# Kernel optimization log

Hardware: AMD Instinct MI355X
Metric: run time of the kernel (lower is better)

## Reference

```python
import jax, jax.numpy as jnp
import numpy as np
import math

MUL = 16                      # num_in_features == num_out_features
LDIMS = (1, 3, 5)             # 0e, 1o, 2e  (lmax = 2)
FEAT = MUL * sum(LDIMS)       # 144 = irreps dim = number_of_basis
PATHS = [(0,0,0),(1,1,0),(2,2,0),
         (0,1,1),(1,0,1),(1,2,1),(2,1,1),
         (0,2,2),(1,1,2),(2,0,2),(2,2,2)]
DOT_PATHS = [(0,0,0),(1,1,0),(2,2,0)]

# ---------- real Wigner-3j / Clebsch-Gordan (e3nn convention), numpy precompute ----------

def _su2_cg(j1, m1, j2, m2, j3, m3):
    if m3 != m1 + m2:
        return 0.0
    f = math.factorial
    vmin = max(-j1 + j2 + m3, -j1 + m1, 0)
    vmax = min(j2 + j3 + m1, j3 - j1 + j2, j3 + m3)
    C = math.sqrt((2*j3+1) * f(j3+j1-j2) * f(j3-j1+j2) * f(j1+j2-j3)
                  * f(j3+m3) * f(j3-m3)
                  / (f(j1+j2+j3+1) * f(j1-m1) * f(j1+m1) * f(j2-m2) * f(j2+m2)))
    S = 0.0
    for v in range(vmin, vmax + 1):
        S += (-1.0)**(v + j2 + m2) * f(j2+j3+m1-v) * f(j1-m1+v) / (
            f(v) * f(j3-j1+j2-v) * f(j3+m3-v) * f(v+j1-j2-m3))
    return C * S

def _qmat(l):
    # complex -> real spherical-harmonic change of basis (e3nn convention)
    q = np.zeros((2*l+1, 2*l+1), dtype=np.complex128)
    for m in range(-l, 0):
        q[l+m, l+abs(m)] = 1.0/math.sqrt(2)
        q[l+m, l-abs(m)] = -1j/math.sqrt(2)
    q[l, l] = 1.0
    for m in range(1, l+1):
        q[l+m, l+abs(m)] = (-1)**m/math.sqrt(2)
        q[l+m, l-abs(m)] = 1j*(-1)**m/math.sqrt(2)
    return (-1j)**l * q

def _real_w3j(l1, l2, l3):
    C = np.zeros((2*l1+1, 2*l2+1, 2*l3+1))
    for i, m1 in enumerate(range(-l1, l1+1)):
        for j, m2 in enumerate(range(-l2, l2+1)):
            for k, m3 in enumerate(range(-l3, l3+1)):
                C[i, j, k] = _su2_cg(l1, m1, l2, m2, l3, m3)
    Cr = np.einsum('ij,kl,mn,ikn->jlm', _qmat(l1), _qmat(l2),
                   np.conj(_qmat(l3).T), C.astype(np.complex128))
    Cr = np.real(Cr)
    return (Cr / np.linalg.norm(Cr)).astype(np.float32)  # unit Frobenius norm (3j convention)

W3J = {p: _real_w3j(*p) for p in set(PATHS)}

# ---------- fully connected tensor product (component/element normalization) ----------

def _split(x):
    # blocked layout: [mul x 0e | mul x 1o | mul x 2e]
    n = x.shape[0]
    xs, o = [], 0
    for d in LDIMS:
        xs.append(x[:, o:o + MUL*d].reshape(n, MUL, d))
        o += MUL * d
    return xs

def _fctp(x1, x2, W):
    # W: [11, u, v, w] stacked per PATHS
    xs1, xs2 = _split(x1), _split(x2)
    n = x1.shape[0]
    n_paths = {l3: sum(1 for p in PATHS if p[2] == l3) for l3 in range(3)}
    outs = [None, None, None]
    for i, (l1, l2, l3) in enumerate(PATHS):
        C = jnp.asarray(W3J[(l1, l2, l3)])          # [i, j, k]
        scale = math.sqrt((2*l3 + 1) / (n_paths[l3] * MUL * MUL))
        a = jnp.einsum('nvj,ijk->nivk', xs2[l2], C)      # [n, i, v, k]
        b = jnp.einsum('nui,nivk->nuvk', xs1[l1], a)     # [n, u, v, k]
        o = scale * jnp.einsum('nuvk,uvw->nwk', b, W[i]) # [n, w, k]
        outs[l3] = o if outs[l3] is None else outs[l3] + o
    return jnp.concatenate([o.reshape(n, -1) for o in outs], axis=1)  # [n, 9*MUL]

def _dot(x1, x2, Wd):
    # FCTP(irreps_input, irreps_input, '0e'): paths (0,0,0),(1,1,0),(2,2,0), out mul = 1
    xs1, xs2 = _split(x1), _split(x2)
    fan = 3 * MUL * MUL
    acc = 0.0
    for i, (l1, l2, l3) in enumerate(DOT_PATHS):
        C = jnp.asarray(W3J[(l1, l2, l3)])[:, :, 0]      # [i, j]
        t = jnp.einsum('nui,ij,nvj->nuv', xs1[l1], C, xs2[l2])
        acc = acc + jnp.einsum('nuv,uv->n', t, Wd[i])
    return (acc * math.sqrt(1.0 / fan))[:, None]         # [n, 1]

def setup_inputs() -> dict:
    key = jax.random.key(0)
    ks = jax.random.split(key, 8)
    N = 50000
    return {
        'nodes_features': jax.random.normal(ks[0], (N, FEAT), jnp.float32),
        'degree_matrix': jax.random.normal(ks[1], (N,), jnp.float32),
        'edges_features_distance': jax.random.normal(ks[2], (N,), jnp.float32),
        'edges_features_bond': jax.random.normal(ks[3], (N,), jnp.float32),
        'w_q': jax.random.normal(ks[4], (11, MUL, MUL, MUL), jnp.float32),
        'w_k': jax.random.normal(ks[5], (11, MUL, MUL, MUL), jnp.float32),
        'w_v': jax.random.normal(ks[6], (11, MUL, MUL, MUL), jnp.float32),
        'w_dot': jax.random.normal(ks[7], (3, MUL, MUL), jnp.float32),
    }

def reference(nodes_features, degree_matrix, edges_features_distance,
              edges_features_bond, w_q, w_k, w_v, w_dot):
    # degree_matrix / edges_features_* are unused by the original forward
    x = nodes_features
    q = _fctp(x, x, w_q)                   # tp_q(x, x)
    k = _fctp(x, x, w_k)                   # tp_k(x, x)
    v = _fctp(x, x, w_v)                   # tp(x, x)
    d = _dot(q, k, w_dot)                  # [n, 1]
    e = jnp.exp(d / math.sqrt(float(FEAT)))
    attn = e / (e + 1e-10)                 # sum over last dim of size 1 + eps
    out = attn * v                         # dropout is identity in eval mode
    out = out.reshape(-1, MUL)             # view(-1, num_heads * num_out_features)
    return jax.nn.elu(out)                 # [9n, MUL]
```

## Files before the change

kernel.cpp:

```cpp
#include <hip/hip_runtime.h>
#include <math.h>

#define NP 11
#define NN 8

__device__ __constant__ int g_l1[NP]   = {0,1,2,0,1,1,2,0,1,2,2};
__device__ __constant__ int g_l2[NP]   = {0,1,2,1,0,2,1,2,1,0,2};
__device__ __constant__ int g_l3[NP]   = {0,0,0,1,1,1,1,2,2,2,2};
__device__ __constant__ int g_coff[NP] = {0,1,10,35,44,53,98,143,168,213,238};

typedef _Float16 half8 __attribute__((ext_vector_type(8)));
typedef _Float16 h2 __attribute__((ext_vector_type(2)));
typedef float f32x4 __attribute__((ext_vector_type(4)));

__device__ __forceinline__ float bfu(unsigned int v){ return __uint_as_float(v<<16); }
__device__ __forceinline__ unsigned int rne16(float f){
  unsigned int ui=__float_as_uint(f);
  return (ui+0x7fffu+((ui>>16)&1u))>>16;
}
__device__ __forceinline__ unsigned short h16(float f){
  _Float16 h=(_Float16)f;
  return __builtin_bit_cast(unsigned short,h);
}

__device__ double dfact(int n){ double r=1.0; for(int i=2;i<=n;++i) r*=(double)i; return r; }

__device__ double su2_cg(int j1,int m1,int j2,int m2,int j3,int m3){
  if(m1+m2!=m3) return 0.0;
  int vmin=-j1+j2+m3; if(-j1+m1>vmin) vmin=-j1+m1; if(vmin<0) vmin=0;
  int vmax=j2+j3+m1; int t=j3-j1+j2; if(t<vmax) vmax=t; t=j3+m3; if(t<vmax) vmax=t;
  double C = sqrt((double)(2*j3+1)*dfact(j3+j1-j2)*dfact(j3-j1+j2)*dfact(j1+j2-j3)
      *dfact(j3+m3)*dfact(j3-m3)
      /(dfact(j1+j2+j3+1)*dfact(j1-m1)*dfact(j1+m1)*dfact(j2-m2)*dfact(j2+m2)));
  double S=0.0;
  for(int v=vmin;v<=vmax;++v){
    double sg = ((v+j2+m2)&1)? -1.0:1.0;
    S += sg*dfact(j2+j3+m1-v)*dfact(j1-m1+v)
        /(dfact(v)*dfact(j3-j1+j2-v)*dfact(j3+m3-v)*dfact(v+j1-j2-m3));
  }
  return C*S;
}

__device__ void qelem(int l,int r,int c,double &re,double &im){
  int m=r-l; double a=0.0,b=0.0; const double s=0.70710678118654752440;
  if(m<0){ if(c==l-m) a=s; else if(c==l+m) b=-s; }
  else if(m==0){ if(c==l) a=1.0; }
  else { double sg=(m&1)?-1.0:1.0; if(c==l+m) a=sg*s; else if(c==l-m) b=sg*s; }
  if(l==1){ double tt=a; a=b; b=-tt; }
  else if(l==2){ a=-a; b=-b; }
  re=a; im=b;
}

__device__ int probe_f32(const unsigned short* __restrict__ p, int nelem, int* scnt){
  if(threadIdx.x==0) *scnt=0;
  __syncthreads();
  int M = nelem < 4096 ? nelem : 4096;
  int c=0;
  for(int t=threadIdx.x;t<M;t+=blockDim.x){
    unsigned e=((unsigned)p[t]>>7)&0xFFu;
    if(e!=0u && (e<0x70u || e>0x8Eu)) ++c;
  }
  atomicAdd(scnt,c);
  __syncthreads();
  return (*scnt*8 > M) ? 1 : 0;
}

__global__ void prep(const unsigned short* __restrict__ x,
                     const unsigned short* __restrict__ wq,
                     const unsigned short* __restrict__ wk,
                     const unsigned short* __restrict__ wv,
                     const unsigned short* __restrict__ wd,
                     int nx,int nw,int nd,
                     float* __restrict__ c3j, unsigned int* __restrict__ cgh,
                     unsigned int* __restrict__ wpre){
  const int p=blockIdx.x, tp=blockIdx.y;
  __shared__ double cg[125];
  __shared__ double outv[125];
  __shared__ double nrm;
  __shared__ int scnt;

  const unsigned short* ww=(tp==0)?wq:((tp==1)?wk:wv);
  const int f32 = probe_f32(ww,nw,&scnt);

  {
    unsigned int* dst=wpre+(size_t)(p*3+tp)*2240;
    for(int t=threadIdx.x;t<2048;t+=256){
      int w=t>>7, c=t&127;
      int i0=c*32+w, i1=i0+16;
      float f0,f1;
      if(f32){
        const float* wf=(const float*)ww+(size_t)p*4096;
        f0=wf[i0]; f1=wf[i1];
      }else{
        const unsigned short* wsp=ww+(size_t)p*4096;
        f0=bfu(wsp[i0]); f1=bfu(wsp[i1]);
      }
      dst[w*140+c]=(unsigned int)h16(f0)|((unsigned int)h16(f1)<<16);
    }
  }

  if(tp==0){
    int l1=g_l1[p], l2=g_l2[p], l3=g_l3[p];
    int d1=2*l1+1, d2=2*l2+1, d3=2*l3+1;
    int tot=d1*d2*d3;
    for(int t=threadIdx.x;t<tot;t+=256){
      int i=t/(d2*d3), k=(t/d3)%d2, n=t%d3;
      cg[t]=su2_cg(l1,i-l1,l2,k-l2,l3,n-l3);
    }
    __syncthreads();
    for(int t=threadIdx.x;t<tot;t+=256){
      int a=t/(d2*d3), b=(t/d3)%d2, c=t%d3;
      double sre=0.0;
      for(int i=0;i<d1;++i){ double q1r,q1i; qelem(l1,i,a,q1r,q1i);
        for(int k=0;k<d2;++k){ double q2r,q2i; qelem(l2,k,b,q2r,q2i);
          double pr=q1r*q2r-q1i*q2i, pi=q1r*q2i+q1i*q2r;
          for(int n=0;n<d3;++n){ double q3r,q3i; qelem(l3,n,c,q3r,q3i);
            sre += (pr*q3r + pi*q3i) * cg[(i*d2+k)*d3+n];
          }
        }
      }
      outv[t]=sre;
    }
    __syncthreads();
    if(threadIdx.x==0){
      double s=0.0; for(int t=0;t<tot;++t) s+=outv[t]*outv[t];
      nrm=sqrt(s);
    }
    __syncthreads();
    const float scl_[3]={0.03608439182435161f,0.05412658773652741f,0.06987712429686843f};
    float s=scl_[l3];
    for(int t=threadIdx.x;t<tot;t+=256){
      float val=(float)(outv[t]/nrm);
      c3j[g_coff[p]+t]=val;
      unsigned int h=(unsigned int)h16(val*s);
      cgh[g_coff[p]+t]=h|(h<<16);
    }
  }

  if(p==0 && tp==0){
    int xf=probe_f32(x,nx,&scnt);
    if(threadIdx.x==0) c3j[363]=(float)xf;
    int df=probe_f32(wd,nd,&scnt);
    if(threadIdx.x==0) c3j[367]=(float)df;
  }
}

template<int D1,int D2,int D3>
__device__ __forceinline__ void fusedAB(const unsigned int* __restrict__ sXp,
                                        const unsigned int* __restrict__ sXd,
                                        const unsigned int* __restrict__ cgp,
                                        unsigned int* __restrict__ sAu,
                                        int wave, int lane, int nvalid){
  constexpr int O1=(D1==1)?0:((D1==3)?16:64);
  constexpr int O2P=(D2==1)?0:((D2==3)?8:32);
  const int nn=lane>>3, vp=lane&7;
  if(nn>=nvalid) return;
  h2 x2p[D2];
  #pragma unroll
  for(int j=0;j<D2;++j) x2p[j]=__builtin_bit_cast(h2,sXp[nn*76+O2P+vp*D2+j]);
  const int u0=wave*2;
  h2 x1a[D1],x1b[D1];
  #pragma unroll
  for(int i=0;i<D1;++i){
    x1a[i]=__builtin_bit_cast(h2,sXd[nn*148+O1+u0*D1+i]);
    x1b[i]=__builtin_bit_cast(h2,sXd[nn*148+O1+(u0+1)*D1+i]);
  }
  h2 acc0[D3],acc1[D3];
  #pragma unroll
  for(int k=0;k<D3;++k){ acc0[k]=(h2){(_Float16)0.f,(_Float16)0.f}; acc1[k]=acc0[k]; }
  #pragma unroll
  for(int i=0;i<D1;++i){
    #pragma unroll
    for(int k=0;k<D3;++k){
      h2 ar=(h2){(_Float16)0.f,(_Float16)0.f};
      #pragma unroll
      for(int j=0;j<D2;++j)
        ar+=__builtin_bit_cast(h2,cgp[(i*D2+j)*D3+k])*x2p[j];
      acc0[k]+=x1a[i]*ar;
      acc1[k]+=x1b[i]*ar;
    }
  }
  #pragma unroll
  for(int k=0;k<D3;++k){
    sAu[(k*8+nn)*140+u0*8+vp]   =__builtin_bit_cast(unsigned int,acc0[k]);
    sAu[(k*8+nn)*140+u0*8+vp+8] =__builtin_bit_cast(unsigned int,acc1[k]);
  }
}

template<int L3>
__device__ __forceinline__ void stage2_acc(const unsigned int* __restrict__ sAu,
                                           const unsigned int* __restrict__ wp_path,
                                           const uint4* __restrict__ bf,
                                           f32x4& a0, f32x4& a1,
                                           int n16, int quad, int wave){
  constexpr int P=(L3+1)*3;
  if(wave<P){
    int Mt=wave/3;
    const unsigned int* ap=sAu+(Mt*16+n16)*140+quad*4;
    f32x4 a=a0;
    #pragma unroll
    for(int ks=0;ks<8;++ks)
      a=__builtin_amdgcn_mfma_f32_16x16x32_f16(
          *reinterpret_cast<const half8*>(ap+ks*16),
          __builtin_bit_cast(half8,bf[ks]),a,0,0,0);
    a0=a;
  }
  if(L3==2 && wave==0){
    const unsigned int* ap=sAu+(2*16+n16)*140+quad*4;
    const uint4* bp=(const uint4*)(wp_path+2*2240+n16*140+quad*4);
    uint4 b2[8];
    #pragma unroll
    for(int ks=0;ks<8;++ks) b2[ks]=bp[ks*4];
    f32x4 a=a1;
    #pragma unroll
    for(int ks=0;ks<8;++ks)
      a=__builtin_amdgcn_mfma_f32_16x16x32_f16(
          *reinterpret_cast<const half8*>(ap+ks*16),
          __builtin_bit_cast(half8,b2[ks]),a,0,0,0);
    a1=a;
  }
}

template<int L3>
__device__ __forceinline__ void stage2_out(const f32x4& a0, const f32x4& a1,
                                           float* __restrict__ sO,
                                           int n16, int quad, int wave){
  constexpr int D3=2*L3+1;
  constexpr int OO=(L3==0)?0:((L3==1)?16:64);
  constexpr int P=(L3+1)*3;
  if(wave<P){
    int tp=wave%3, Mt=wave/3;
    #pragma unroll
    for(int reg=0;reg<4;++reg){
      int row=Mt*16+quad*4+reg;
      int k=row>>3, node=row&7;
      if(k<D3) sO[node*440+tp*144+OO+n16*D3+k]=a0[reg];
    }
  }
  if(L3==2 && wave==0){
    #pragma unroll
    for(int reg=0;reg<4;++reg){
      int row=32+quad*4+reg;
      int k=row>>3, node=row&7;
      if(k<D3) sO[node*440+2*144+OO+n16*D3+k]=a1[reg];
    }
  }
}

__global__ __launch_bounds__(512,6) void tfn_main(
    const unsigned short* __restrict__ xin,
    const unsigned int* __restrict__ wpre,
    const unsigned int* __restrict__ cgh,
    const unsigned short* __restrict__ wd,
    const float* __restrict__ c3j,
    unsigned short* __restrict__ outp, int N)
{
  __shared__ __align__(16) unsigned int sAu[48*140];
  __shared__ float sO[NN*440];
  __shared__ __align__(8) unsigned int sXp[NN*76];
  __shared__ __align__(8) unsigned int sXd[NN*148];
  __shared__ float sWd[768];

  const int tid=threadIdx.x;
  const int wave=tid>>6, lane=tid&63;
  const int n16=lane&15, quad=lane>>4;
  const int node0=blockIdx.x*NN;
  const int nvalid=(N-node0)<NN?(N-node0):NN;

  const int xf32 = c3j[363]!=0.0f;
  const int df32 = c3j[367]!=0.0f;

  float* scratch=sO;
  if(!xf32){
    for(int t=tid;t<NN*36;t+=512){
      int nn=t/36, w4=t%36;
      if(nn<nvalid){
        uint2 u=((const uint2*)(xin+(size_t)(node0+nn)*144))[w4];
        float* dst=&scratch[nn*144+w4*4];
        dst[0]=bfu(u.x&0xffffu); dst[1]=bfu(u.x>>16);
        dst[2]=bfu(u.y&0xffffu); dst[3]=bfu(u.y>>16);
      }
    }
  }else{
    const float* xf=(const float*)xin;
    for(int t=tid;t<NN*144;t+=512){
      int nn=t/144, f=t%144;
      if(nn<nvalid) scratch[nn*144+f]=xf[(size_t)(node0+nn)*144+f];
    }
  }
  if(!df32){ for(int t=tid;t<768;t+=512) sWd[t]=bfu((unsigned int)wd[t]); }
  else     { const float* wdf=(const float*)wd; for(int t=tid;t<768;t+=512) sWd[t]=wdf[t]; }
  __syncthreads();

  for(int t=tid;t<NN*144;t+=512){
    int nn=t/144, f=t-nn*144;
    unsigned int h=(unsigned int)h16(scratch[t]);
    sXd[nn*148+f]=h|(h<<16);
  }
  for(int t=tid;t<NN*72;t+=512){
    int nn=t/72, g=t-nn*72;
    int fa,fb;
    if(g<8){ fa=2*g; fb=fa+1; }
    else if(g<32){ int gg=g-8; int vp=gg/3, j=gg-3*vp; fa=16+(2*vp)*3+j; fb=fa+3; }
    else { int gg=g-32; int vp=gg/5, j=gg-5*vp; fa=64+(2*vp)*5+j; fb=fa+5; }
    sXp[nn*76+g]=(unsigned int)h16(scratch[nn*144+fa])|((unsigned int)h16(scratch[nn*144+fb])<<16);
  }
  __syncthreads();

  #define PATH_STEP(P_,D1_,D2_,D3_) { \
    const int PT=((D3_-1)/2+1)*3; \
    uint4 bf[8]; \
    if(wave<PT){ \
      const uint4* bp=(const uint4*)(wpre+(size_t)P_*6720+(wave%3)*2240+n16*140+quad*4); \
      bf[0]=bp[0];  bf[1]=bp[4];  bf[2]=bp[8];  bf[3]=bp[12]; \
      bf[4]=bp[16]; bf[5]=bp[20]; bf[6]=bp[24]; bf[7]=bp[28]; \
    } \
    fusedAB<D1_,D2_,D3_>(sXp,sXd,cgh+g_coff[P_],sAu,wave,lane,nvalid); \
    __syncthreads(); \
    stage2_acc<(D3_-1)/2>(sAu,wpre+(size_t)P_*6720,bf,a0,a1,n16,quad,wave); \
    __syncthreads(); }

  {
    f32x4 a0={0.f,0.f,0.f,0.f}, a1={0.f,0.f,0.f,0.f};
    PATH_STEP(0,1,1,1)
    PATH_STEP(1,3,3,1)
    PATH_STEP(2,5,5,1)
    stage2_out<0>(a0,a1,sO,n16,quad,wave);
  }
  {
    f32x4 a0={0.f,0.f,0.f,0.f}, a1={0.f,0.f,0.f,0.f};
    PATH_STEP(3,1,3,3)
    PATH_STEP(4,3,1,3)
    PATH_STEP(5,3,5,3)
    PATH_STEP(6,5,3,3)
    stage2_out<1>(a0,a1,sO,n16,quad,wave);
  }
  {
    f32x4 a0={0.f,0.f,0.f,0.f}, a1={0.f,0.f,0.f,0.f};
    PATH_STEP(7,1,5,5)
    PATH_STEP(8,3,3,5)
    PATH_STEP(9,5,1,5)
    PATH_STEP(10,5,5,5)
    stage2_out<2>(a0,a1,sO,n16,quad,wave);
  }
  #undef PATH_STEP
  __syncthreads();

  {
    int node=wave;
    if(node<nvalid){
      const float c0=c3j[0], c1=c3j[1], c2=c3j[10];
      const float* qv=sO+node*440;
      const float* kv=qv+144;
      const int v=lane&15, ug=lane>>4;
      float k0=kv[v];
      float k1[3],k2[5];
      #pragma unroll
      for(int j=0;j<3;++j) k1[j]=kv[16+v*3+j];
      #pragma unroll
      for(int m=0;m<5;++m) k2[m]=kv[64+v*5+m];
      float part=0.f;
      #pragma unroll
      for(int t=0;t<4;++t){
        int u=ug+4*t;
        float d0=qv[u]*k0;
        float d1=0.f;
        #pragma unroll
        for(int j=0;j<3;++j) d1+=qv[16+u*3+j]*k1[j];
        float d2=0.f;
        #pragma unroll
        for(int m=0;m<5;++m) d2+=qv[64+u*5+m]*k2[m];
        part+=sWd[u*16+v]*(c0*d0)+sWd[256+u*16+v]*(c1*d1)+sWd[512+u*16+v]*(c2*d2);
      }
      #pragma unroll
      for(int off=1;off<64;off<<=1) part+=__shfl_xor(part,off,64);
      float dd=part*0.03608439182435161f;
      float ex=dd*(1.0f/12.0f);
      ex=fminf(fmaxf(ex,-80.f),80.f);
      float e=expf(ex);
      float attn=e/(e+1e-10f);
      const float* vv=sO+node*440+288;
      if(!xf32){
        unsigned short* ob=outp+(size_t)(node0+node)*144;
        for(int f=lane;f<144;f+=64){
          float val=attn*vv[f];
          float r=(val>0.f)?val:expm1f(val);
          ob[f]=(unsigned short)rne16(r);
        }
      }else{
        float* ob=(float*)outp+(size_t)(node0+node)*144;
        for(int f=lane;f<144;f+=64){
          float val=attn*vv[f];
          ob[f]=(val>0.f)?val:expm1f(val);
        }
      }
    }
  }
}

extern "C" void kernel_launch(void* const* d_in, const int* in_sizes, int n_in,
                              void* d_out, int out_size, void* d_ws, size_t ws_size,
                              hipStream_t stream){
  (void)n_in; (void)out_size; (void)ws_size;
  const unsigned short* x =(const unsigned short*)d_in[0];
  const unsigned short* wq=(const unsigned short*)d_in[4];
  const unsigned short* wk=(const unsigned short*)d_in[5];
  const unsigned short* wv=(const unsigned short*)d_in[6];
  const unsigned short* wd=(const unsigned short*)d_in[7];
  float* c3j=(float*)d_ws;
  unsigned int* cgh=(unsigned int*)d_ws+1024;
  unsigned int* wpre=(unsigned int*)d_ws+2048;
  int N=in_sizes[0]/144;
  prep<<<dim3(NP,3),dim3(256),0,stream>>>(x,wq,wk,wv,wd,
      in_sizes[0],in_sizes[4],in_sizes[7],c3j,cgh,wpre);
  int nb=(N+NN-1)/NN;
  tfn_main<<<dim3(nb),dim3(512),0,stream>>>(x,wpre,cgh,wd,c3j,(unsigned short*)d_out,N);
}
```

Measured before the change: 355.6 us.

## Restructure TFN kernel: 64 nodes per block, per-wave register MFMA, staged weights

Reworks the main kernel so each 256-thread block handles 64 nodes, one 16-node tile per wave. The CG-contracted intermediate is built directly in registers as the MFMA B operand, and q, k and v are computed in one pass with shared weight tiles. Per-path weights are staged in LDS and the next path is prefetched into registers while the current one computes, so weight traffic is amortised over 64 nodes instead of 8. The q·k dot product is done with cross-lane shuffles from accumulators instead of an LDS round trip. In exchange, register pressure rises (q, k and v accumulators for up to five components each), occupancy is limited by the launch bound of 256 threads with 2 blocks, and there are more block-wide barriers per path.

Measured after the change: 428.3 us. 20.4% more time.

```diff
diff --git a/kernel.cpp b/kernel.cpp
--- a/kernel.cpp
+++ b/kernel.cpp
@@ -2,7 +2,6 @@
 #include <math.h>
 
 #define NP 11
-#define NN 8
 
 __device__ __constant__ int g_l1[NP]   = {0,1,2,0,1,1,2,0,1,2,2};
 __device__ __constant__ int g_l2[NP]   = {0,1,2,1,0,2,1,2,1,0,2};
@@ -146,108 +145,108 @@
 }
 
 template<int D1,int D2,int D3>
-__device__ __forceinline__ void fusedAB(const unsigned int* __restrict__ sXp,
-                                        const unsigned int* __restrict__ sXd,
+__device__ __forceinline__ void do_path(const unsigned int* __restrict__ xrow,
+                                        const unsigned int* __restrict__ wbase,
                                         const unsigned int* __restrict__ cgp,
-                                        unsigned int* __restrict__ sAu,
-                                        int wave, int lane, int nvalid){
-  constexpr int O1=(D1==1)?0:((D1==3)?16:64);
-  constexpr int O2P=(D2==1)?0:((D2==3)?8:32);
-  const int nn=lane>>3, vp=lane&7;
-  if(nn>=nvalid) return;
-  h2 x2p[D2];
+                                        f32x4 (&aq)[D3], f32x4 (&ak)[D3], f32x4 (&av)[D3],
+                                        int hsel, int bsel)
+{
+  constexpr int O1=(D1==1)?0:((D1==3)?8:32);
+  constexpr int O2=(D2==1)?0:((D2==3)?8:32);
+  constexpr int KC=(4*D1*D3<=48)?D3:(48/(4*D1));
+  h2 x2p[4][D2];
+  {
+    const int vb=O2+4*hsel*D2;
+    #pragma unroll
+    for(int e=0;e<4;++e)
+      #pragma unroll
+      for(int j=0;j<D2;++j)
+        x2p[e][j]=__builtin_bit_cast(h2,xrow[vb+e*D2+j]);
+  }
   #pragma unroll
-  for(int j=0;j<D2;++j) x2p[j]=__builtin_bit_cast(h2,sXp[nn*76+O2P+vp*D2+j]);
-  const int u0=wave*2;
-  h2 x1a[D1],x1b[D1];
+  for(int k0=0;k0<D3;k0+=KC){
+    h2 ar[KC][D1][4];
+    #pragma unroll
+    for(int kk=0;kk<KC;++kk){
+      if(k0+kk<D3){
+        #pragma unroll
+        for(int i=0;i<D1;++i){
+          #pragma unroll
+          for(int e=0;e<4;++e){
+            h2 s={(_Float16)0.f,(_Float16)0.f};
+            #pragma unroll
+            for(int j=0;j<D2;++j)
+              s+=__builtin_bit_cast(h2,cgp[(i*D2+j)*D3+(k0+kk)])*x2p[e][j];
+            ar[kk][i][e]=s;
+          }
+        }
+      }
+    }
+    for(int s=0;s<8;++s){
+      uint4 wq4=*(const uint4*)(wbase+s*16);
+      uint4 wk4=*(const uint4*)(wbase+2240+s*16);
+      uint4 wv4=*(const uint4*)(wbase+4480+s*16);
+      h2 x1d[D1];
+      #pragma unroll
+      for(int i=0;i<D1;++i){
+        unsigned int X=xrow[O1+s*D1+i];
+        unsigned int lo=X&0xffffu, hi=X>>16;
+        unsigned int d=bsel?(hi|(hi<<16)):(lo|(lo<<16));
+        x1d[i]=__builtin_bit_cast(h2,d);
+      }
+      #pragma unroll
+      for(int kk=0;kk<KC;++kk){
+        if(k0+kk<D3){
+          h2 b0={(_Float16)0.f,(_Float16)0.f},b1=b0,b2=b0,b3=b0;
+          #pragma unroll
+          for(int i=0;i<D1;++i){
+            b0+=x1d[i]*ar[kk][i][0];
+            b1+=x1d[i]*ar[kk][i][1];
+            b2+=x1d[i]*ar[kk][i][2];
+            b3+=x1d[i]*ar[kk][i][3];
+          }
+          uint4 bu;
+          bu.x=__builtin_bit_cast(unsigned int,b0);
+          bu.y=__builtin_bit_cast(unsigned int,b1);
+          bu.z=__builtin_bit_cast(unsigned int,b2);
+          bu.w=__builtin_bit_cast(unsigned int,b3);
+          half8 B=__builtin_bit_cast(half8,bu);
+          aq[k0+kk]=__builtin_amdgcn_mfma_f32_16x16x32_f16(__builtin_bit_cast(half8,wq4),B,aq[k0+kk],0,0,0);
+          ak[k0+kk]=__builtin_amdgcn_mfma_f32_16x16x32_f16(__builtin_bit_cast(half8,wk4),B,ak[k0+kk],0,0,0);
+          av[k0+kk]=__builtin_amdgcn_mfma_f32_16x16x32_f16(__builtin_bit_cast(half8,wv4),B,av[k0+kk],0,0,0);
+        }
+      }
+    }
+  }
+}
+
+template<int D3>
+__device__ __forceinline__ float dot_group(const f32x4 (&aq)[D3], const f32x4 (&ak)[D3],
+                                           const float* __restrict__ sWd_l,
+                                           int nd, int qp)
+{
+  float P=0.f;
   #pragma unroll
-  for(int i=0;i<D1;++i){
-    x1a[i]=__builtin_bit_cast(h2,sXd[nn*148+O1+u0*D1+i]);
-    x1b[i]=__builtin_bit_cast(h2,sXd[nn*148+O1+(u0+1)*D1+i]);
-  }
-  h2 acc0[D3],acc1[D3];
-  #pragma unroll
-  for(int k=0;k<D3;++k){ acc0[k]=(h2){(_Float16)0.f,(_Float16)0.f}; acc1[k]=acc0[k]; }
-  #pragma unroll
-  for(int i=0;i<D1;++i){
-    #pragma unroll
-    for(int k=0;k<D3;++k){
-      h2 ar=(h2){(_Float16)0.f,(_Float16)0.f};
-      #pragma unroll
-      for(int j=0;j<D2;++j)
-        ar+=__builtin_bit_cast(h2,cgp[(i*D2+j)*D3+k])*x2p[j];
-      acc0[k]+=x1a[i]*ar;
-      acc1[k]+=x1b[i]*ar;
-    }
-  }
-  #pragma unroll
-  for(int k=0;k<D3;++k){
-    sAu[(k*8+nn)*140+u0*8+vp]   =__builtin_bit_cast(unsigned int,acc0[k]);
-    sAu[(k*8+nn)*140+u0*8+vp+8] =__builtin_bit_cast(unsigned int,acc1[k]);
-  }
-}
-
-template<int L3>
-__device__ __forceinline__ void stage2_acc(const unsigned int* __restrict__ sAu,
-                                           const unsigned int* __restrict__ wp_path,
-                                           const uint4* __restrict__ bf,
-                                           f32x4& a0, f32x4& a1,
-                                           int n16, int quad, int wave){
-  constexpr int P=(L3+1)*3;
-  if(wave<P){
-    int Mt=wave/3;
-    const unsigned int* ap=sAu+(Mt*16+n16)*140+quad*4;
-    f32x4 a=a0;
-    #pragma unroll
-    for(int ks=0;ks<8;++ks)
-      a=__builtin_amdgcn_mfma_f32_16x16x32_f16(
-          *reinterpret_cast<const half8*>(ap+ks*16),
-          __builtin_bit_cast(half8,bf[ks]),a,0,0,0);
-    a0=a;
-  }
-  if(L3==2 && wave==0){
-    const unsigned int* ap=sAu+(2*16+n16)*140+quad*4;
-    const uint4* bp=(const uint4*)(wp_path+2*2240+n16*140+quad*4);
-    uint4 b2[8];
-    #pragma unroll
-    for(int ks=0;ks<8;++ks) b2[ks]=bp[ks*4];
-    f32x4 a=a1;
-    #pragma unroll
-    for(int ks=0;ks<8;++ks)
-      a=__builtin_amdgcn_mfma_f32_16x16x32_f16(
-          *reinterpret_cast<const half8*>(ap+ks*16),
-          __builtin_bit_cast(half8,b2[ks]),a,0,0,0);
-    a1=a;
-  }
-}
-
-template<int L3>
-__device__ __forceinline__ void stage2_out(const f32x4& a0, const f32x4& a1,
-                                           float* __restrict__ sO,
-                                           int n16, int quad, int wave){
-  constexpr int D3=2*L3+1;
-  constexpr int OO=(L3==0)?0:((L3==1)?16:64);
-  constexpr int P=(L3+1)*3;
-  if(wave<P){
-    int tp=wave%3, Mt=wave/3;
-    #pragma unroll
-    for(int reg=0;reg<4;++reg){
-      int row=Mt*16+quad*4+reg;
-      int k=row>>3, node=row&7;
-      if(k<D3) sO[node*440+tp*144+OO+n16*D3+k]=a0[reg];
-    }
-  }
-  if(L3==2 && wave==0){
-    #pragma unroll
-    for(int reg=0;reg<4;++reg){
-      int row=32+quad*4+reg;
-      int k=row>>3, node=row&7;
-      if(k<D3) sO[node*440+2*144+OO+n16*D3+k]=a1[reg];
-    }
-  }
-}
-
-__global__ __launch_bounds__(512,6) void tfn_main(
+  for(int v=0;v<16;++v){
+    float kv[D3];
+    const int src=nd+((v>>2)<<4);
+    #pragma unroll
+    for(int m=0;m<D3;++m) kv[m]=__shfl(ak[m][v&3],src,64);
+    #pragma unroll
+    for(int r=0;r<4;++r){
+      float dm=0.f;
+      #pragma unroll
+      for(int m=0;m<D3;++m) dm+=aq[m][r]*kv[m];
+      P+=sWd_l[(4*qp+r)*16+v]*dm;
+    }
+  }
+  return P;
+}
+
+#define XPOFF 9216
+#define WDOFF 14144
+
+__global__ __launch_bounds__(256,2) void tfn_main(
     const unsigned short* __restrict__ xin,
     const unsigned int* __restrict__ wpre,
     const unsigned int* __restrict__ cgh,
@@ -255,144 +254,179 @@
     const float* __restrict__ c3j,
     unsigned short* __restrict__ outp, int N)
 {
-  __shared__ __align__(16) unsigned int sAu[48*140];
-  __shared__ float sO[NN*440];
-  __shared__ __align__(8) unsigned int sXp[NN*76];
-  __shared__ __align__(8) unsigned int sXd[NN*148];
-  __shared__ float sWd[768];
+  __shared__ __align__(16) unsigned int SM[14912];
 
   const int tid=threadIdx.x;
-  const int wave=tid>>6, lane=tid&63;
-  const int n16=lane&15, quad=lane>>4;
-  const int node0=blockIdx.x*NN;
-  const int nvalid=(N-node0)<NN?(N-node0):NN;
+  const int lane=tid&63, wave=tid>>6;
+  const int nd=lane&15, qp=lane>>4;
+  const int hsel=qp&1, bsel=qp>>1;
+  const int nl=wave*16+nd;
+  const int node0=blockIdx.x*64;
+  const int nvalid=(N-node0)<64?(N-node0):64;
 
   const int xf32 = c3j[363]!=0.0f;
   const int df32 = c3j[367]!=0.0f;
-
-  float* scratch=sO;
+  const float c0=c3j[0], c1=c3j[1], c2=c3j[10];
+
+  uint4 ws[7];
+  #define W_LOAD(PN) { \
+    const uint4* wsrc=(const uint4*)(wpre+(size_t)(PN)*6720); \
+    _Pragma("unroll") \
+    for(int r=0;r<6;++r) ws[r]=wsrc[tid+256*r]; \
+    if(tid<144) ws[6]=wsrc[tid+1536]; }
+  #define W_STORE() { \
+    uint4* wl=(uint4*)SM; \
+    _Pragma("unroll") \
+    for(int r=0;r<6;++r) wl[tid+256*r]=ws[r]; \
+    if(tid<144) wl[tid+1536]=ws[6]; }
+
+  W_LOAD(0)
+
   if(!xf32){
-    for(int t=tid;t<NN*36;t+=512){
-      int nn=t/36, w4=t%36;
-      if(nn<nvalid){
-        uint2 u=((const uint2*)(xin+(size_t)(node0+nn)*144))[w4];
-        float* dst=&scratch[nn*144+w4*4];
-        dst[0]=bfu(u.x&0xffffu); dst[1]=bfu(u.x>>16);
-        dst[2]=bfu(u.y&0xffffu); dst[3]=bfu(u.y>>16);
-      }
+    const uint4* xsrc=(const uint4*)(xin+(size_t)node0*144);
+    for(int idx=tid;idx<1152;idx+=256){
+      int node=idx/18;
+      uint4 v={0u,0u,0u,0u};
+      if(node<nvalid) v=xsrc[idx];
+      ((uint4*)SM)[idx]=v;
     }
   }else{
-    const float* xf=(const float*)xin;
-    for(int t=tid;t<NN*144;t+=512){
-      int nn=t/144, f=t%144;
-      if(nn<nvalid) scratch[nn*144+f]=xf[(size_t)(node0+nn)*144+f];
-    }
-  }
-  if(!df32){ for(int t=tid;t<768;t+=512) sWd[t]=bfu((unsigned int)wd[t]); }
-  else     { const float* wdf=(const float*)wd; for(int t=tid;t<768;t+=512) sWd[t]=wdf[t]; }
-  __syncthreads();
-
-  for(int t=tid;t<NN*144;t+=512){
-    int nn=t/144, f=t-nn*144;
-    unsigned int h=(unsigned int)h16(scratch[t]);
-    sXd[nn*148+f]=h|(h<<16);
-  }
-  for(int t=tid;t<NN*72;t+=512){
-    int nn=t/72, g=t-nn*72;
-    int fa,fb;
-    if(g<8){ fa=2*g; fb=fa+1; }
-    else if(g<32){ int gg=g-8; int vp=gg/3, j=gg-3*vp; fa=16+(2*vp)*3+j; fb=fa+3; }
-    else { int gg=g-32; int vp=gg/5, j=gg-5*vp; fa=64+(2*vp)*5+j; fb=fa+5; }
-    sXp[nn*76+g]=(unsigned int)h16(scratch[nn*144+fa])|((unsigned int)h16(scratch[nn*144+fb])<<16);
-  }
-  __syncthreads();
-
-  #define PATH_STEP(P_,D1_,D2_,D3_) { \
-    const int PT=((D3_-1)/2+1)*3; \
-    uint4 bf[8]; \
-    if(wave<PT){ \
-      const uint4* bp=(const uint4*)(wpre+(size_t)P_*6720+(wave%3)*2240+n16*140+quad*4); \
-      bf[0]=bp[0];  bf[1]=bp[4];  bf[2]=bp[8];  bf[3]=bp[12]; \
-      bf[4]=bp[16]; bf[5]=bp[20]; bf[6]=bp[24]; bf[7]=bp[28]; \
-    } \
-    fusedAB<D1_,D2_,D3_>(sXp,sXd,cgh+g_coff[P_],sAu,wave,lane,nvalid); \
+    const uint4* xsrc=(const uint4*)((const float*)xin+(size_t)node0*144);
+    for(int idx=tid;idx<2304;idx+=256){
+      int node=idx/36;
+      uint4 v={0u,0u,0u,0u};
+      if(node<nvalid) v=xsrc[idx];
+      ((uint4*)SM)[idx]=v;
+    }
+  }
+  if(!df32){ for(int t=tid;t<768;t+=256) ((float*)SM)[WDOFF+t]=bfu((unsigned int)wd[t]); }
+  else     { const float* wdf=(const float*)wd; for(int t=tid;t<768;t+=256) ((float*)SM)[WDOFF+t]=wdf[t]; }
+  __syncthreads();
+
+  {
+    const unsigned short* raw16=(const unsigned short*)SM;
+    const float* rawf=(const float*)SM;
+    for(int t=tid;t<64*72;t+=256){
+      int n=t/72, g=t-n*72;
+      int fa,fb;
+      if(g<8){ fa=2*g; fb=fa+1; }
+      else if(g<32){ int gg=g-8; int vp=gg/3, j=gg-3*vp; fa=16+(2*vp)*3+j; fb=fa+3; }
+      else { int gg=g-32; int vp=gg/5, j=gg-5*vp; fa=64+(2*vp)*5+j; fb=fa+5; }
+      float va,vb;
+      if(!xf32){ va=bfu(raw16[n*144+fa]); vb=bfu(raw16[n*144+fb]); }
+      else     { va=rawf[n*144+fa];       vb=rawf[n*144+fb]; }
+      SM[XPOFF+n*77+g]=(unsigned int)h16(va)|((unsigned int)h16(vb)<<16);
+    }
+  }
+  __syncthreads();
+
+  W_STORE()
+  W_LOAD(1)
+  __syncthreads();
+
+  const unsigned int* xrow=SM+XPOFF+nl*77;
+  const unsigned int* wbase=SM+nd*140+qp*4;
+  const float* sWd=(const float*)(SM+WDOFF);
+
+  #define W_SWAP(PN) { \
     __syncthreads(); \
-    stage2_acc<(D3_-1)/2>(sAu,wpre+(size_t)P_*6720,bf,a0,a1,n16,quad,wave); \
+    W_STORE() \
+    if((PN)<11){ W_LOAD(PN) } \
     __syncthreads(); }
 
-  {
-    f32x4 a0={0.f,0.f,0.f,0.f}, a1={0.f,0.f,0.f,0.f};
-    PATH_STEP(0,1,1,1)
-    PATH_STEP(1,3,3,1)
-    PATH_STEP(2,5,5,1)
-    stage2_out<0>(a0,a1,sO,n16,quad,wave);
-  }
-  {
-    f32x4 a0={0.f,0.f,0.f,0.f}, a1={0.f,0.f,0.f,0.f};
-    PATH_STEP(3,1,3,3)
-    PATH_STEP(4,3,1,3)
-    PATH_STEP(5,3,5,3)
-    PATH_STEP(6,5,3,3)
-    stage2_out<1>(a0,a1,sO,n16,quad,wave);
-  }
-  {
-    f32x4 a0={0.f,0.f,0.f,0.f}, a1={0.f,0.f,0.f,0.f};
-    PATH_STEP(7,1,5,5)
-    PATH_STEP(8,3,3,5)
-    PATH_STEP(9,5,1,5)
-    PATH_STEP(10,5,5,5)
-    stage2_out<2>(a0,a1,sO,n16,quad,wave);
-  }
-  #undef PATH_STEP
-  __syncthreads();
-
-  {
-    int node=wave;
-    if(node<nvalid){
-      const float c0=c3j[0], c1=c3j[1], c2=c3j[10];
-      const float* qv=sO+node*440;
-      const float* kv=qv+144;
-      const int v=lane&15, ug=lane>>4;
-      float k0=kv[v];
-      float k1[3],k2[5];
-      #pragma unroll
-      for(int j=0;j<3;++j) k1[j]=kv[16+v*3+j];
-      #pragma unroll
-      for(int m=0;m<5;++m) k2[m]=kv[64+v*5+m];
-      float part=0.f;
-      #pragma unroll
-      for(int t=0;t<4;++t){
-        int u=ug+4*t;
-        float d0=qv[u]*k0;
-        float d1=0.f;
-        #pragma unroll
-        for(int j=0;j<3;++j) d1+=qv[16+u*3+j]*k1[j];
-        float d2=0.f;
-        #pragma unroll
-        for(int m=0;m<5;++m) d2+=qv[64+u*5+m]*k2[m];
-        part+=sWd[u*16+v]*(c0*d0)+sWd[256+u*16+v]*(c1*d1)+sWd[512+u*16+v]*(c2*d2);
-      }
-      #pragma unroll
-      for(int off=1;off<64;off<<=1) part+=__shfl_xor(part,off,64);
-      float dd=part*0.03608439182435161f;
-      float ex=dd*(1.0f/12.0f);
-      ex=fminf(fmaxf(ex,-80.f),80.f);
-      float e=expf(ex);
-      float attn=e/(e+1e-10f);
-      const float* vv=sO+node*440+288;
-      if(!xf32){
-        unsigned short* ob=outp+(size_t)(node0+node)*144;
-        for(int f=lane;f<144;f+=64){
-          float val=attn*vv[f];
-          float r=(val>0.f)?val:expm1f(val);
-          ob[f]=(unsigned short)rne16(r);
-        }
-      }else{
-        float* ob=(float*)outp+(size_t)(node0+node)*144;
-        for(int f=lane;f<144;f+=64){
-          float val=attn*vv[f];
-          ob[f]=(val>0.f)?val:expm1f(val);
-        }
+  const f32x4 z4={0.f,0.f,0.f,0.f};
+  f32x4 av0[1]={z4};
+  f32x4 av1[3]={z4,z4,z4};
+  f32x4 av2[5]={z4,z4,z4,z4,z4};
+  float dd=0.f;
+
+  {
+    f32x4 aq[1]={z4}, ak[1]={z4};
+    do_path<1,1,1>(xrow,wbase,cgh+0 ,aq,ak,av0,hsel,bsel);
+    W_SWAP(2)
+    do_path<3,3,1>(xrow,wbase,cgh+1 ,aq,ak,av0,hsel,bsel);
+    W_SWAP(3)
+    do_path<5,5,1>(xrow,wbase,cgh+10,aq,ak,av0,hsel,bsel);
+    W_SWAP(4)
+    dd+=c0*dot_group<1>(aq,ak,sWd,nd,qp);
+  }
+  {
+    f32x4 aq[3]={z4,z4,z4}, ak[3]={z4,z4,z4};
+    do_path<1,3,3>(xrow,wbase,cgh+35,aq,ak,av1,hsel,bsel);
+    W_SWAP(5)
+    do_path<3,1,3>(xrow,wbase,cgh+44,aq,ak,av1,hsel,bsel);
+    W_SWAP(6)
+    do_path<3,5,3>(xrow,wbase,cgh+53,aq,ak,av1,hsel,bsel);
+    W_SWAP(7)
+    do_path<5,3,3>(xrow,wbase,cgh+98,aq,ak,av1,hsel,bsel);
+    W_SWAP(8)
+    dd+=c1*dot_group<3>(aq,ak,sWd+256,nd,qp);
+  }
+  {
+    f32x4 aq[5]={z4,z4,z4,z4,z4}, ak[5]={z4,z4,z4,z4,z4};
+    do_path<1,5,5>(xrow,wbase,cgh+143,aq,ak,av2,hsel,bsel);
+    W_SWAP(9)
+    do_path<3,3,5>(xrow,wbase,cgh+168,aq,ak,av2,hsel,bsel);
+    W_SWAP(10)
+    do_path<5,1,5>(xrow,wbase,cgh+213,aq,ak,av2,hsel,bsel);
+    W_SWAP(11)
+    do_path<5,5,5>(xrow,wbase,cgh+238,aq,ak,av2,hsel,bsel);
+    dd+=c2*dot_group<5>(aq,ak,sWd+512,nd,qp);
+  }
+  #undef W_SWAP
+  #undef W_LOAD
+  #undef W_STORE
+
+  dd+=__shfl_xor(dd,16,64);
+  dd+=__shfl_xor(dd,32,64);
+  float ex=dd*0.03608439182435161f*(1.0f/12.0f);
+  ex=fminf(fmaxf(ex,-80.f),80.f);
+  float e=expf(ex);
+  float attn=e/(e+1e-10f);
+
+  __syncthreads();
+
+  {
+    float* row=(float*)SM+nl*148;
+    #pragma unroll
+    for(int r=0;r<4;++r){
+      float v=attn*av0[0][r];
+      row[4*qp+r]=(v>0.f)?v:expm1f(v);
+    }
+    #pragma unroll
+    for(int m=0;m<3;++m)
+      #pragma unroll
+      for(int r=0;r<4;++r){
+        float v=attn*av1[m][r];
+        row[16+(4*qp+r)*3+m]=(v>0.f)?v:expm1f(v);
+      }
+    #pragma unroll
+    for(int m=0;m<5;++m)
+      #pragma unroll
+      for(int r=0;r<4;++r){
+        float v=attn*av2[m][r];
+        row[64+(4*qp+r)*5+m]=(v>0.f)?v:expm1f(v);
+      }
+  }
+  __syncthreads();
+
+  const float* img=(const float*)SM;
+  if(!xf32){
+    unsigned int* ob=(unsigned int*)outp;
+    for(int t=tid;t<64*72;t+=256){
+      int n=t/72, fp=t-n*72;
+      if(n<nvalid){
+        float v0=img[n*148+2*fp], v1=img[n*148+2*fp+1];
+        ob[(size_t)(node0+n)*72+fp]=rne16(v0)|(rne16(v1)<<16);
+      }
+    }
+  }else{
+    float* outf=(float*)outp;
+    for(int t=tid;t<64*36;t+=256){
+      int n=t/36, c=t-n*36;
+      if(n<nvalid){
+        uint4 v=*(const uint4*)(img+n*148+c*4);
+        *((uint4*)(outf+(size_t)(node0+n)*144)+c)=v;
       }
     }
   }
@@ -413,6 +447,6 @@
   int N=in_sizes[0]/144;
   prep<<<dim3(NP,3),dim3(256),0,stream>>>(x,wq,wk,wv,wd,
       in_sizes[0],in_sizes[4],in_sizes[7],c3j,cgh,wpre);
-  int nb=(N+NN-1)/NN;
-  tfn_main<<<dim3(nb),dim3(512),0,stream>>>(x,wpre,cgh,wd,c3j,(unsigned short*)d_out,N);
-}
+  int nb=(N+63)/64;
+  tfn_main<<<dim3(nb),dim3(256),0,stream>>>(x,wpre,cgh,wd,c3j,(unsigned short*)d_out,N);
+}
```
